# Kernel optimization log

Hardware: AMD Instinct MI355X
Metric: run time of the kernel (lower is better)

Reference implementation:

```python
import jax, jax.numpy as jnp
import numpy as np

K = 3  # hardcoded in TransitionUp.forward

def setup_inputs() -> dict:
    key = jax.random.key(0)
    ks = jax.random.split(key, 8)
    M, N = 32768, 8192
    UP_C, DOWN_C, OUT_C = 128, 256, 128
    return {
        "up_points": jax.random.normal(ks[0], (M, 3), dtype=jnp.float32),
        "up_features": jax.random.normal(ks[1], (M, UP_C), dtype=jnp.float32),
        "down_points": jax.random.normal(ks[2], (N, 3), dtype=jnp.float32),
        "down_features": jax.random.normal(ks[3], (N, DOWN_C), dtype=jnp.float32),
        # torch nn.Linear params: W [out,in], b [out]
        "W_up": jax.random.normal(ks[4], (OUT_C, UP_C), dtype=jnp.float32) / np.sqrt(UP_C),
        "b_up": jax.random.normal(ks[5], (OUT_C,), dtype=jnp.float32) * 0.01,
        "W_down": jax.random.normal(ks[6], (OUT_C, DOWN_C), dtype=jnp.float32) / np.sqrt(DOWN_C),
        "b_down": jax.random.normal(ks[7], (OUT_C,), dtype=jnp.float32) * 0.01,
    }

def interpolate_knn(query_points, dataset_points, dataset_features, k):
    # squared pairwise distances [M, N]
    delta = query_points[:, None, :] - dataset_points[None, :, :]
    dist = jnp.sum(delta * delta, axis=-1)
    neg_dist, knn_idx = jax.lax.top_k(-dist, k)  # smallest-k
    knn_dist = -neg_dist                           # [M, k]
    knn_feats = dataset_features[knn_idx]          # [M, k, C]
    recip = 1.0 / (knn_dist + 1e-8)
    weights = recip / jnp.sum(recip, axis=-1, keepdims=True)  # [M, k]
    return jnp.einsum('mk,mkc->mc', weights, knn_feats)

def reference(up_points, up_features, down_points, down_features, W_up, b_up, W_down, b_down):
    down_f = down_features @ W_down.T + b_down            # [N, OUT_C]
    interp_f = interpolate_knn(up_points, down_points, down_f, K)  # [M, OUT_C]
    return interp_f + (up_features @ W_up.T + b_up)
```

## Files before the change

### kernel.cpp

```cpp
#include <hip/hip_runtime.h>
#include <cfloat>

#define M_UP   32768
#define N_DOWN 8192
#define UPC    128
#define DOWNC  256
#define OUTC   128
#define NCHUNK 8
#define CHUNK  (N_DOWN / NCHUNK)
#define G      8
#define Q      2
#define PG     12

__device__ __forceinline__ void fma4(float4& acc, float s, const float4 w) {
    acc.x = fmaf(s, w.x, acc.x);
    acc.y = fmaf(s, w.y, acc.y);
    acc.z = fmaf(s, w.z, acc.z);
    acc.w = fmaf(s, w.w, acc.w);
}

__device__ __forceinline__ void top3_bl(float s, int idx,
                                        float& d0, float& d1, float& d2,
                                        int& i0, int& i1, int& i2) {
    bool c0 = s < d0, c1 = s < d1, c2 = s < d2;
    float n0 = fminf(d0, s);
    float n1 = __builtin_amdgcn_fmed3f(d0, d1, s);
    float n2 = __builtin_amdgcn_fmed3f(d1, d2, s);
    int m0 = c0 ? idx : i0;
    int m1 = c0 ? i0 : (c1 ? idx : i1);
    int m2 = c1 ? i1 : (c2 ? idx : i2);
    d0 = n0; d1 = n1; d2 = n2;
    i0 = m0; i1 = m1; i2 = m2;
}

__global__ __launch_bounds__(256) void transpose_w(
        const float* __restrict__ W_up, const float* __restrict__ W_down,
        float* __restrict__ wt_up, float* __restrict__ wt_down) {
    int e = blockIdx.x * 256 + threadIdx.x;
    if (e < DOWNC * OUTC) {
        int k = e >> 7, c = e & 127;
        wt_down[e] = W_down[c * DOWNC + k];
    } else {
        int e2 = e - DOWNC * OUTC;
        int k = e2 >> 7, c = e2 & 127;
        wt_up[e2] = W_up[c * UPC + k];
    }
}

template <int K>
__device__ __forceinline__ void gemm_tile32(
        const float* __restrict__ A, const float* __restrict__ WT,
        float* sA , float* sW ,
        int rbase, int tid, float4 acc[2][2]) {
    const int rl = tid & 15;
    const int c0 = (tid >> 4) * 8;
    #pragma unroll 1
    for (int ph = 0; ph < K / 32; ++ph) {
        if (ph) __syncthreads();
        {
            int r = tid >> 3, k4 = tid & 7;
            float4 v = *(const float4*)(A + (size_t)(rbase + r) * K + ph * 32 + k4 * 4);
            *(float4*)&sA[r * 36 + k4 * 4] = v;
        }
        #pragma unroll
        for (int i = 0; i < 4; ++i) {
            int idx = tid + i * 256;
            int kk = idx >> 5, cc = idx & 31;
            float4 v = *(const float4*)(WT + (size_t)(ph * 32 + kk) * OUTC + cc * 4);
            *(float4*)&sW[kk * OUTC + cc * 4] = v;
        }
        __syncthreads();
        #pragma unroll 4
        for (int kk = 0; kk < 32; ++kk) {
            float a0 = sA[rl * 36 + kk];
            float a1 = sA[(rl + 16) * 36 + kk];
            float4 w0 = *(const float4*)&sW[kk * OUTC + c0];
            float4 w1 = *(const float4*)&sW[kk * OUTC + c0 + 4];
            fma4(acc[0][0], a0, w0); fma4(acc[0][1], a0, w1);
            fma4(acc[1][0], a1, w0); fma4(acc[1][1], a1, w1);
        }
    }
}

__global__ __launch_bounds__(256) void down_proj(
        const float* __restrict__ A, const float* __restrict__ WT,
        const float* __restrict__ bias, float* __restrict__ down_f) {
    __shared__ __align__(16) float sA[32 * 36];
    __shared__ __align__(16) float sW[32 * OUTC];
    float4 acc[2][2] = {};
    gemm_tile32<DOWNC>(A, WT, sA, sW, blockIdx.x * 32, threadIdx.x, acc);
    const int rl = threadIdx.x & 15;
    const int cg = (threadIdx.x >> 4) * 2;
    const float4 b0 = ((const float4*)bias)[cg];
    const float4 b1 = ((const float4*)bias)[cg + 1];
    #pragma unroll
    for (int i = 0; i < 2; ++i) {
        const int row = blockIdx.x * 32 + rl + 16 * i;
        float4 v0 = acc[i][0], v1 = acc[i][1];
        v0.x += b0.x; v0.y += b0.y; v0.z += b0.z; v0.w += b0.w;
        v1.x += b1.x; v1.y += b1.y; v1.z += b1.z; v1.w += b1.w;
        ((float4*)down_f)[row * 32 + cg] = v0;
        ((float4*)down_f)[row * 32 + cg + 1] = v1;
    }
}

__global__ __launch_bounds__(256) void knn_partial(
        const float* __restrict__ up_points,
        const float* __restrict__ down_points,
        float2* __restrict__ part) {
    __shared__ __align__(16) float sx[PG * (CHUNK / G)];
    __shared__ __align__(16) float sy[PG * (CHUNK / G)];
    __shared__ __align__(16) float sz[PG * (CHUNK / G)];
    const int base = blockIdx.y * CHUNK;
    for (int t = threadIdx.x; t < CHUNK; t += 256) {
        int g = base + t;
        int gi = t >> 3, j = t & 7;
        sx[PG * gi + j] = down_points[3 * g];
        sy[PG * gi + j] = down_points[3 * g + 1];
        sz[PG * gi + j] = down_points[3 * g + 2];
    }
    __syncthreads();

    const int m0 = blockIdx.x * (256 * Q) + threadIdx.x;
    const int m1 = m0 + 256;
    const float q0x = up_points[3 * m0];
    const float q0y = up_points[3 * m0 + 1];
    const float q0z = up_points[3 * m0 + 2];
    const float q1x = up_points[3 * m1];
    const float q1y = up_points[3 * m1 + 1];
    const float q1z = up_points[3 * m1 + 2];

    float a_gd0 = FLT_MAX, a_gd1 = FLT_MAX, a_gd2 = FLT_MAX;
    int   a_gi0 = 0, a_gi1 = 0, a_gi2 = 0;
    float b_gd0 = FLT_MAX, b_gd1 = FLT_MAX, b_gd2 = FLT_MAX;
    int   b_gi0 = 0, b_gi1 = 0, b_gi2 = 0;

    for (int gi = 0; gi < CHUNK / G; ++gi) {
        float4 x0 = *(const float4*)&sx[PG * gi], x1 = *(const float4*)&sx[PG * gi + 4];
        float4 y0 = *(const float4*)&sy[PG * gi], y1 = *(const float4*)&sy[PG * gi + 4];
        float4 z0 = *(const float4*)&sz[PG * gi], z1 = *(const float4*)&sz[PG * gi + 4];
        float px[G] = {x0.x, x0.y, x0.z, x0.w, x1.x, x1.y, x1.z, x1.w};
        float py[G] = {y0.x, y0.y, y0.z, y0.w, y1.x, y1.y, y1.z, y1.w};
        float pz[G] = {z0.x, z0.y, z0.z, z0.w, z1.x, z1.y, z1.z, z1.w};
        float s0[G], s1[G];
        #pragma unroll
        for (int j = 0; j < G; ++j) {
            float dx0 = q0x - px[j], dy0 = q0y - py[j], dz0 = q0z - pz[j];
            s0[j] = fmaf(dz0, dz0, fmaf(dy0, dy0, dx0 * dx0));
            float dx1 = q1x - px[j], dy1 = q1y - py[j], dz1 = q1z - pz[j];
            s1[j] = fmaf(dz1, dz1, fmaf(dy1, dy1, dx1 * dx1));
        }
        float gm0 = fminf(fminf(fminf(s0[0], s0[1]), fminf(s0[2], s0[3])),
                          fminf(fminf(s0[4], s0[5]), fminf(s0[6], s0[7])));
        float gm1 = fminf(fminf(fminf(s1[0], s1[1]), fminf(s1[2], s1[3])),
                          fminf(fminf(s1[4], s1[5]), fminf(s1[6], s1[7])));
        top3_bl(gm0, gi, a_gd0, a_gd1, a_gd2, a_gi0, a_gi1, a_gi2);
        top3_bl(gm1, gi, b_gd0, b_gd1, b_gd2, b_gi0, b_gi1, b_gi2);
    }

    #pragma unroll
    for (int qq = 0; qq < Q; ++qq) {
        const float qx = qq ? q1x : q0x;
        const float qy = qq ? q1y : q0y;
        const float qz = qq ? q1z : q0z;
        int bases[3];
        if (qq == 0) { bases[0] = a_gi0; bases[1] = a_gi1; bases[2] = a_gi2; }
        else         { bases[0] = b_gi0; bases[1] = b_gi1; bases[2] = b_gi2; }
        float D0 = FLT_MAX, D1 = FLT_MAX, D2 = FLT_MAX;
        int I0 = 0, I1 = 0, I2 = 0;
        #pragma unroll
        for (int t = 0; t < 3; ++t) {
            const int gb = bases[t];
            float4 x0 = *(const float4*)&sx[PG * gb], x1 = *(const float4*)&sx[PG * gb + 4];
            float4 y0 = *(const float4*)&sy[PG * gb], y1 = *(const float4*)&sy[PG * gb + 4];
            float4 z0 = *(const float4*)&sz[PG * gb], z1 = *(const float4*)&sz[PG * gb + 4];
            float px[G] = {x0.x, x0.y, x0.z, x0.w, x1.x, x1.y, x1.z, x1.w};
            float py[G] = {y0.x, y0.y, y0.z, y0.w, y1.x, y1.y, y1.z, y1.w};
            float pz[G] = {z0.x, z0.y, z0.z, z0.w, z1.x, z1.y, z1.z, z1.w};
            #pragma unroll
            for (int j = 0; j < G; ++j) {
                float dx = qx - px[j], dy = qy - py[j], dz = qz - pz[j];
                float s = fmaf(dz, dz, fmaf(dy, dy, dx * dx));
                top3_bl(s, base + gb * G + j, D0, D1, D2, I0, I1, I2);
            }
        }
        const int m = qq ? m1 : m0;
        const int o = (blockIdx.y * M_UP + m) * 3;
        part[o]     = make_float2(D0, __int_as_float(I0));
        part[o + 1] = make_float2(D1, __int_as_float(I1));
        part[o + 2] = make_float2(D2, __int_as_float(I2));
    }
}

__global__ __launch_bounds__(256) void up_fused(
        const float* __restrict__ A, const float* __restrict__ WT,
        const float* __restrict__ bias, const float* __restrict__ down_f,
        const float2* __restrict__ part,
        float* __restrict__ out) {
    __shared__ __align__(16) float sA[32 * 36];
    __shared__ __align__(16) float sW[32 * OUTC];
    float4 acc[2][2] = {};
    gemm_tile32<UPC>(A, WT, sA, sW, blockIdx.x * 32, threadIdx.x, acc);

    const int rl = threadIdx.x & 15;
    const int cg = (threadIdx.x >> 4) * 2;
    const float4 b0 = ((const float4*)bias)[cg];
    const float4 b1 = ((const float4*)bias)[cg + 1];
    const float4* df4 = (const float4*)down_f;
    #pragma unroll
    for (int i = 0; i < 2; ++i) {
        const int m = blockIdx.x * 32 + rl + 16 * i;
        float D0 = FLT_MAX, D1 = FLT_MAX, D2 = FLT_MAX;
        int I0 = 0, I1 = 0, I2 = 0;
        #pragma unroll
        for (int s = 0; s < NCHUNK; ++s) {
            const float2* p = part + (s * M_UP + m) * 3;
            #pragma unroll
            for (int j = 0; j < 3; ++j) {
                float2 v = p[j];
                top3_bl(v.x, __float_as_int(v.y), D0, D1, D2, I0, I1, I2);
            }
        }
        float r0 = 1.f / (D0 + 1e-8f);
        float r1 = 1.f / (D1 + 1e-8f);
        float r2 = 1.f / (D2 + 1e-8f);
        float rs = (r0 + r1) + r2;
        float w0 = r0 / rs, w1 = r1 / rs, w2 = r2 / rs;
        float4 f00 = df4[I0 * 32 + cg],     f01 = df4[I0 * 32 + cg + 1];
        float4 f10 = df4[I1 * 32 + cg],     f11 = df4[I1 * 32 + cg + 1];
        float4 f20 = df4[I2 * 32 + cg],     f21 = df4[I2 * 32 + cg + 1];
        float4 v0 = acc[i][0], v1 = acc[i][1];
        float4 res0, res1;
        res0.x = v0.x + b0.x + fmaf(w0, f00.x, fmaf(w1, f10.x, w2 * f20.x));
        res0.y = v0.y + b0.y + fmaf(w0, f00.y, fmaf(w1, f10.y, w2 * f20.y));
        res0.z = v0.z + b0.z + fmaf(w0, f00.z, fmaf(w1, f10.z, w2 * f20.z));
        res0.w = v0.w + b0.w + fmaf(w0, f00.w, fmaf(w1, f10.w, w2 * f20.w));
        res1.x = v1.x + b1.x + fmaf(w0, f01.x, fmaf(w1, f11.x, w2 * f21.x));
        res1.y = v1.y + b1.y + fmaf(w0, f01.y, fmaf(w1, f11.y, w2 * f21.y));
        res1.z = v1.z + b1.z + fmaf(w0, f01.z, fmaf(w1, f11.z, w2 * f21.z));
        res1.w = v1.w + b1.w + fmaf(w0, f01.w, fmaf(w1, f11.w, w2 * f21.w));
        ((float4*)out)[m * 32 + cg] = res0;
        ((float4*)out)[m * 32 + cg + 1] = res1;
    }
}

extern "C" void kernel_launch(void* const* d_in, const int* in_sizes, int n_in,
                              void* d_out, int out_size, void* d_ws, size_t ws_size,
                              hipStream_t stream) {
    const float* up_points     = (const float*)d_in[0];
    const float* up_features   = (const float*)d_in[1];
    const float* down_points   = (const float*)d_in[2];
    const float* down_features = (const float*)d_in[3];
    const float* W_up          = (const float*)d_in[4];
    const float* b_up          = (const float*)d_in[5];
    const float* W_down        = (const float*)d_in[6];
    const float* b_down        = (const float*)d_in[7];
    float* out = (float*)d_out;

    float* wt_down = (float*)d_ws;
    float* wt_up   = wt_down + DOWNC * OUTC;
    float* down_f  = wt_up + UPC * OUTC;
    float2* part   = (float2*)(down_f + N_DOWN * OUTC);

    transpose_w<<<(DOWNC * OUTC + UPC * OUTC) / 256, 256, 0, stream>>>(
        W_up, W_down, wt_up, wt_down);
    down_proj<<<N_DOWN / 32, 256, 0, stream>>>(
        down_features, wt_down, b_down, down_f);
    knn_partial<<<dim3(M_UP / (256 * Q), NCHUNK), 256, 0, stream>>>(
        up_points, down_points, part);
    up_fused<<<M_UP / 32, 256, 0, stream>>>(
        up_features, wt_up, b_up, down_f, part, out);
}
```

Measured before the change: 188.2 us.

## Retile up_fused GEMM to 128-row blocks with 8x8 register tiles

```diff
diff --git a/kernel.cpp b/kernel.cpp
--- a/kernel.cpp
+++ b/kernel.cpp
@@ -192,56 +192,116 @@
     }
 }
 
-__global__ __launch_bounds__(256) void up_fused(
+__device__ __forceinline__ void up_row_epilogue(
+        int m, int ct, float4 a0, float4 a1,
+        const float4 b0, const float4 b1,
+        const float2* __restrict__ part, const float4* __restrict__ df4,
+        float4* __restrict__ out4) {
+    float D0 = FLT_MAX, D1 = FLT_MAX, D2 = FLT_MAX;
+    int I0 = 0, I1 = 0, I2 = 0;
+    #pragma unroll
+    for (int s = 0; s < NCHUNK; ++s) {
+        const float2* p = part + ((size_t)s * M_UP + m) * 3;
+        float2 v0 = p[0], v1 = p[1], v2 = p[2];
+        top3_bl(v0.x, __float_as_int(v0.y), D0, D1, D2, I0, I1, I2);
+        top3_bl(v1.x, __float_as_int(v1.y), D0, D1, D2, I0, I1, I2);
+        top3_bl(v2.x, __float_as_int(v2.y), D0, D1, D2, I0, I1, I2);
+    }
+    float r0 = 1.f / (D0 + 1e-8f);
+    float r1 = 1.f / (D1 + 1e-8f);
+    float r2 = 1.f / (D2 + 1e-8f);
+    float rs = (r0 + r1) + r2;
+    float w0 = r0 / rs, w1 = r1 / rs, w2 = r2 / rs;
+    float4 f00 = df4[I0 * 32 + ct],      f01 = df4[I0 * 32 + ct + 16];
+    float4 f10 = df4[I1 * 32 + ct],      f11 = df4[I1 * 32 + ct + 16];
+    float4 f20 = df4[I2 * 32 + ct],      f21 = df4[I2 * 32 + ct + 16];
+    float4 res0, res1;
+    res0.x = a0.x + b0.x + fmaf(w0, f00.x, fmaf(w1, f10.x, w2 * f20.x));
+    res0.y = a0.y + b0.y + fmaf(w0, f00.y, fmaf(w1, f10.y, w2 * f20.y));
+    res0.z = a0.z + b0.z + fmaf(w0, f00.z, fmaf(w1, f10.z, w2 * f20.z));
+    res0.w = a0.w + b0.w + fmaf(w0, f00.w, fmaf(w1, f10.w, w2 * f20.w));
+    res1.x = a1.x + b1.x + fmaf(w0, f01.x, fmaf(w1, f11.x, w2 * f21.x));
+    res1.y = a1.y + b1.y + fmaf(w0, f01.y, fmaf(w1, f11.y, w2 * f21.y));
+    res1.z = a1.z + b1.z + fmaf(w0, f01.z, fmaf(w1, f11.z, w2 * f21.z));
+    res1.w = a1.w + b1.w + fmaf(w0, f01.w, fmaf(w1, f11.w, w2 * f21.w));
+    out4[m * 32 + ct] = res0;
+    out4[m * 32 + ct + 16] = res1;
+}
+
+__global__ __launch_bounds__(256, 1) void up_fused(
         const float* __restrict__ A, const float* __restrict__ WT,
         const float* __restrict__ bias, const float* __restrict__ down_f,
         const float2* __restrict__ part,
         float* __restrict__ out) {
-    __shared__ __align__(16) float sA[32 * 36];
-    __shared__ __align__(16) float sW[32 * OUTC];
-    float4 acc[2][2] = {};
-    gemm_tile32<UPC>(A, WT, sA, sW, blockIdx.x * 32, threadIdx.x, acc);
-
-    const int rl = threadIdx.x & 15;
-    const int cg = (threadIdx.x >> 4) * 2;
-    const float4 b0 = ((const float4*)bias)[cg];
-    const float4 b1 = ((const float4*)bias)[cg + 1];
+    __shared__ __align__(16) float sAT[32][128];
+    __shared__ __align__(16) float sW[32][128];
+    const int tid = threadIdx.x;
+    const int rt8 = (tid >> 4) * 8;
+    const int ct  = tid & 15;
+    const int ct4 = ct * 4;
+    const int rbase = blockIdx.x * 128;
+
+    float4 acc[8][2] = {};
+    #pragma unroll 1
+    for (int ph = 0; ph < UPC / 32; ++ph) {
+        if (ph) __syncthreads();
+        {
+            int r = tid >> 1;
+            int kb = (tid & 1) * 16;
+            const float* Ar = A + (size_t)(rbase + r) * UPC + ph * 32 + kb;
+            #pragma unroll
+            for (int i = 0; i < 4; ++i) {
+                float4 v = *(const float4*)(Ar + i * 4);
+                int k0 = kb + i * 4;
+                sAT[k0][r] = v.x; sAT[k0 + 1][r] = v.y;
+                sAT[k0 + 2][r] = v.z; sAT[k0 + 3][r] = v.w;
+            }
+        }
+        {
+            const float4* Wp = (const float4*)(WT + (size_t)ph * 32 * OUTC);
+            float4* sW4 = (float4*)&sW[0][0];
+            #pragma unroll
+            for (int i = 0; i < 4; ++i)
+                sW4[tid + i * 256] = Wp[tid + i * 256];
+        }
+        __syncthreads();
+        #pragma unroll 4
+        for (int kk = 0; kk < 32; ++kk) {
+            float4 aLo = *(const float4*)&sAT[kk][rt8];
+            float4 aHi = *(const float4*)&sAT[kk][rt8 + 4];
+            float4 w0  = *(const float4*)&sW[kk][ct4];
+            float4 w1  = *(const float4*)&sW[kk][64 + ct4];
+            fma4(acc[0][0], aLo.x, w0); fma4(acc[0][1], aLo.x, w1);
+            fma4(acc[1][0], aLo.y, w0); fma4(acc[1][1], aLo.y, w1);
+            fma4(acc[2][0], aLo.z, w0); fma4(acc[2][1], aLo.z, w1);
+            fma4(acc[3][0], aLo.w, w0); fma4(acc[3][1], aLo.w, w1);
+            fma4(acc[4][0], aHi.x, w0); fma4(acc[4][1], aHi.x, w1);
+            fma4(acc[5][0], aHi.y, w0); fma4(acc[5][1], aHi.y, w1);
+            fma4(acc[6][0], aHi.z, w0); fma4(acc[6][1], aHi.z, w1);
+            fma4(acc[7][0], aHi.w, w0); fma4(acc[7][1], aHi.w, w1);
+        }
+    }
+
+    const float4 b0 = ((const float4*)bias)[ct];
+    const float4 b1 = ((const float4*)bias)[ct + 16];
     const float4* df4 = (const float4*)down_f;
-    #pragma unroll
-    for (int i = 0; i < 2; ++i) {
-        const int m = blockIdx.x * 32 + rl + 16 * i;
-        float D0 = FLT_MAX, D1 = FLT_MAX, D2 = FLT_MAX;
-        int I0 = 0, I1 = 0, I2 = 0;
-        #pragma unroll
-        for (int s = 0; s < NCHUNK; ++s) {
-            const float2* p = part + (s * M_UP + m) * 3;
-            #pragma unroll
-            for (int j = 0; j < 3; ++j) {
-                float2 v = p[j];
-                top3_bl(v.x, __float_as_int(v.y), D0, D1, D2, I0, I1, I2);
-            }
-        }
-        float r0 = 1.f / (D0 + 1e-8f);
-        float r1 = 1.f / (D1 + 1e-8f);
-        float r2 = 1.f / (D2 + 1e-8f);
-        float rs = (r0 + r1) + r2;
-        float w0 = r0 / rs, w1 = r1 / rs, w2 = r2 / rs;
-        float4 f00 = df4[I0 * 32 + cg],     f01 = df4[I0 * 32 + cg + 1];
-        float4 f10 = df4[I1 * 32 + cg],     f11 = df4[I1 * 32 + cg + 1];
-        float4 f20 = df4[I2 * 32 + cg],     f21 = df4[I2 * 32 + cg + 1];
-        float4 v0 = acc[i][0], v1 = acc[i][1];
-        float4 res0, res1;
-        res0.x = v0.x + b0.x + fmaf(w0, f00.x, fmaf(w1, f10.x, w2 * f20.x));
-        res0.y = v0.y + b0.y + fmaf(w0, f00.y, fmaf(w1, f10.y, w2 * f20.y));
-        res0.z = v0.z + b0.z + fmaf(w0, f00.z, fmaf(w1, f10.z, w2 * f20.z));
-        res0.w = v0.w + b0.w + fmaf(w0, f00.w, fmaf(w1, f10.w, w2 * f20.w));
-        res1.x = v1.x + b1.x + fmaf(w0, f01.x, fmaf(w1, f11.x, w2 * f21.x));
-        res1.y = v1.y + b1.y + fmaf(w0, f01.y, fmaf(w1, f11.y, w2 * f21.y));
-        res1.z = v1.z + b1.z + fmaf(w0, f01.z, fmaf(w1, f11.z, w2 * f21.z));
-        res1.w = v1.w + b1.w + fmaf(w0, f01.w, fmaf(w1, f11.w, w2 * f21.w));
-        ((float4*)out)[m * 32 + cg] = res0;
-        ((float4*)out)[m * 32 + cg + 1] = res1;
-    }
+    float4* out4 = (float4*)out;
+    const int m0 = rbase + rt8;
+    up_row_epilogue(m0 + 0, ct, acc[0][0], acc[0][1], b0, b1, part, df4, out4);
+    __builtin_amdgcn_sched_barrier(0);
+    up_row_epilogue(m0 + 1, ct, acc[1][0], acc[1][1], b0, b1, part, df4, out4);
+    __builtin_amdgcn_sched_barrier(0);
+    up_row_epilogue(m0 + 2, ct, acc[2][0], acc[2][1], b0, b1, part, df4, out4);
+    __builtin_amdgcn_sched_barrier(0);
+    up_row_epilogue(m0 + 3, ct, acc[3][0], acc[3][1], b0, b1, part, df4, out4);
+    __builtin_amdgcn_sched_barrier(0);
+    up_row_epilogue(m0 + 4, ct, acc[4][0], acc[4][1], b0, b1, part, df4, out4);
+    __builtin_amdgcn_sched_barrier(0);
+    up_row_epilogue(m0 + 5, ct, acc[5][0], acc[5][1], b0, b1, part, df4, out4);
+    __builtin_amdgcn_sched_barrier(0);
+    up_row_epilogue(m0 + 6, ct, acc[6][0], acc[6][1], b0, b1, part, df4, out4);
+    __builtin_amdgcn_sched_barrier(0);
+    up_row_epilogue(m0 + 7, ct, acc[7][0], acc[7][1], b0, b1, part, df4, out4);
 }
 
 extern "C" void kernel_launch(void* const* d_in, const int* in_sizes, int n_in,
@@ -268,6 +328,6 @@
         down_features, wt_down, b_down, down_f);
     knn_partial<<<dim3(M_UP / (256 * Q), NCHUNK), 256, 0, stream>>>(
         up_points, down_points, part);
-    up_fused<<<M_UP / 32, 256, 0, stream>>>(
+    up_fused<<<M_UP / 128, 256, 0, stream>>>(
         up_features, wt_up, b_up, down_f, part, out);
 }
```

Result: slower. 198.5 us (+5.5%).
